# Kernel tuning notes

Hardware: AMD Instinct MI355X
Metric: run time of the kernel (lower is better)

Reference implementation:

```python
import jax, jax.numpy as jnp
import numpy as np

B, S, H, U = 32, 4096, 512, 512


def setup_inputs() -> dict:
    key = jax.random.key(0)
    ks = jax.random.split(key, 6)
    scale = 1.0 / np.sqrt(H)
    return {
        "query": jax.random.normal(ks[0], (B, H), dtype=jnp.float32),
        "values": jax.random.normal(ks[1], (B, S, H), dtype=jnp.float32),
        "W1": jax.random.normal(ks[2], (H, U), dtype=jnp.float32) * scale,
        "b1": jnp.zeros((U,), dtype=jnp.float32),
        "W2": jax.random.normal(ks[3], (H, U), dtype=jnp.float32) * scale,
        "b2": jnp.zeros((U,), dtype=jnp.float32),
        "va": jax.random.normal(ks[4], (U, 1), dtype=jnp.float32) * (1.0 / np.sqrt(U)),
        "bva": jnp.zeros((1,), dtype=jnp.float32),
    }


def reference(query, values, W1, b1, W2, b2, va, bva):
    # query: [B, H] -> [B, 1, U]; values: [B, S, H] -> [B, S, U]
    q_proj = jnp.einsum('bh,hu->bu', query, W1) + b1           # [B, U]
    v_proj = jnp.einsum('bsh,hu->bsu', values, W2) + b2        # [B, S, U]
    scores = jnp.einsum('bsu,uo->bso', jnp.tanh(q_proj[:, None, :] + v_proj), va) + bva  # [B, S, 1]
    attention_weights = jax.nn.softmax(scores, axis=1)         # [B, S, 1]
    context_vector = jnp.sum(attention_weights * values, axis=1)  # [B, H]
    return attention_weights, context_vector
```

## Files before the change

### kernel.cpp

```cpp
#include <hip/hip_runtime.h>
#include <hip/hip_bf16.h>
#include <stdint.h>

#define B_SZ 32
#define S_SZ 4096
#define H_SZ 512
#define U_SZ 512

typedef __attribute__((ext_vector_type(8))) _Float16 half8;
typedef __attribute__((ext_vector_type(4))) float floatx4;

__device__ __forceinline__ void async_copy16(const void* g, void* l) {
    __builtin_amdgcn_global_load_lds(
        (const __attribute__((address_space(1))) void*)g,
        (__attribute__((address_space(3))) void*)l, 16, 0, 0);
}

__global__ __launch_bounds__(256) void prep_kernel(
    const float* __restrict__ W2, _Float16* __restrict__ W2s,
    float* __restrict__ qpb2, float* __restrict__ ctx)
{
    const int t = threadIdx.x;
    const int bid = blockIdx.x;
    const int i = bid * 256 + t;
    const int k = i >> 9, n = i & 511;
    W2s[(k >> 5) * 16384 + ((k >> 3) & 3) * 4096 + n * 8 + (k & 7)] =
        (_Float16)W2[i];
    if (bid < 64) qpb2[i] = 0.0f;
    else if (bid < 128) ctx[(bid - 64) * 256 + t] = 0.0f;
}

__global__ __launch_bounds__(256) void qproj_kernel(
    const float* __restrict__ query, const float* __restrict__ W1,
    const float* __restrict__ b1, const float* __restrict__ b2,
    float* __restrict__ qpb2)
{
    const int b = blockIdx.x, uc = blockIdx.y, ks = blockIdx.z;
    const int u = uc * 256 + threadIdx.x;
    float acc = (ks == 0) ? (b1[u] + b2[u]) : 0.0f;
    const float* q  = query + b * H_SZ + ks * 128;
    const float* Wp = W1 + (size_t)(ks * 128) * U_SZ + u;
    for (int k = 0; k < 128; ++k)
        acc = fmaf(q[k], Wp[(size_t)k * U_SZ], acc);
    atomicAdd(&qpb2[b * U_SZ + u], acc);
}

__global__ __launch_bounds__(256, 2) void scores_kernel(
    const float* __restrict__ values, const _Float16* __restrict__ W2s,
    const float* __restrict__ qpb2, const float* __restrict__ va,
    const float* __restrict__ bva, float* __restrict__ scores)
{
    __shared__ __align__(16) char smem[65536];

    const int t  = threadIdx.x;
    const int w  = t >> 6;
    const int l  = t & 63;
    const int c  = l & 15;
    const int g4 = l >> 4;
    const int m0 = blockIdx.x * 64;
    const int b  = m0 >> 12;

    const float* Abase = values + (size_t)m0 * H_SZ;

    floatx4 acc[4][8];
#pragma unroll
    for (int mt = 0; mt < 4; ++mt)
#pragma unroll
        for (int nt = 0; nt < 8; ++nt) acc[mt][nt] = (floatx4)(0.0f);

    {
        const char* src = (const char*)W2s;
#pragma unroll
        for (int i = 0; i < 8; ++i)
            async_copy16(src + (i * 256 + t) * 16, smem + (i * 256 + t) * 16);
    }
    float4 Apre[4][2];
    {
        const int ko = g4 * 8;
#pragma unroll
        for (int mt = 0; mt < 4; ++mt) {
            const float* ap = Abase + (size_t)(mt * 16 + c) * H_SZ + ko;
            Apre[mt][0] = *(const float4*)(ap);
            Apre[mt][1] = *(const float4*)(ap + 4);
        }
    }
    __syncthreads();

    for (int kb = 0; kb < 16; ++kb) {
        const int cur = kb & 1;
        half8 af[4];
#pragma unroll
        for (int mt = 0; mt < 4; ++mt) {
            half8 a;
            a[0] = (_Float16)Apre[mt][0].x; a[1] = (_Float16)Apre[mt][0].y;
            a[2] = (_Float16)Apre[mt][0].z; a[3] = (_Float16)Apre[mt][0].w;
            a[4] = (_Float16)Apre[mt][1].x; a[5] = (_Float16)Apre[mt][1].y;
            a[6] = (_Float16)Apre[mt][1].z; a[7] = (_Float16)Apre[mt][1].w;
            af[mt] = a;
        }
        if (kb < 15) {
            const int ko = (kb + 1) * 32 + g4 * 8;
#pragma unroll
            for (int mt = 0; mt < 4; ++mt) {
                const float* ap = Abase + (size_t)(mt * 16 + c) * H_SZ + ko;
                Apre[mt][0] = *(const float4*)(ap);
                Apre[mt][1] = *(const float4*)(ap + 4);
            }
            const char* src = (const char*)W2s + (size_t)(kb + 1) * 32768;
            char* dst = smem + (cur ^ 1) * 32768;
#pragma unroll
            for (int i = 0; i < 8; ++i)
                async_copy16(src + (i * 256 + t) * 16, dst + (i * 256 + t) * 16);
        }
        const _Float16* Bc = (const _Float16*)(smem + cur * 32768);
        half8 bf[8];
#pragma unroll
        for (int nt = 0; nt < 8; ++nt)
            bf[nt] = *(const half8*)(Bc + g4 * 4096 + (w * 128 + nt * 16 + c) * 8);
#pragma unroll
        for (int mt = 0; mt < 4; ++mt)
#pragma unroll
            for (int nt = 0; nt < 8; ++nt)
                acc[mt][nt] = __builtin_amdgcn_mfma_f32_16x16x32_f16(
                    af[mt], bf[nt], acc[mt][nt], 0, 0, 0);
        __syncthreads();
    }

    float qv2[8], vv[8], vv2[8];
#pragma unroll
    for (int nt = 0; nt < 8; ++nt) {
        const int n = w * 128 + nt * 16 + c;
        const float q = qpb2[b * U_SZ + n];
        const float v = va[n];
        qv2[nt] = 2.0f * q;
        vv[nt] = v;
        vv2[nt] = 2.0f * v;
    }
    float* red = (float*)smem;
#pragma unroll
    for (int mt = 0; mt < 4; ++mt) {
#pragma unroll
        for (int r = 0; r < 4; ++r) {
            float p = 0.0f;
#pragma unroll
            for (int nt = 0; nt < 8; ++nt) {
                const float ex = __expf(fmaf(acc[mt][nt][r], 2.0f, qv2[nt]));
                const float rc = __builtin_amdgcn_rcpf(ex + 1.0f);
                p = fmaf(-vv2[nt], rc, p + vv[nt]);
            }
            p += __shfl_xor(p, 1);
            p += __shfl_xor(p, 2);
            p += __shfl_xor(p, 4);
            p += __shfl_xor(p, 8);
            if (c == 0) red[(mt * 16 + g4 * 4 + r) * 4 + w] = p;
        }
    }
    __syncthreads();
    if (t < 64)
        scores[m0 + t] = *bva + red[t * 4 + 0] + red[t * 4 + 1] +
                         red[t * 4 + 2] + red[t * 4 + 3];
}

__global__ __launch_bounds__(1024) void sredux_kernel(
    const float* __restrict__ scores, float* __restrict__ ML)
{
    __shared__ float red[16];
    __shared__ float s_max;
    const int b = blockIdx.x;
    const int t = threadIdx.x;
    float4 v = *(const float4*)(scores + b * S_SZ + t * 4);
    float m = fmaxf(fmaxf(v.x, v.y), fmaxf(v.z, v.w));
#pragma unroll
    for (int o = 32; o > 0; o >>= 1) m = fmaxf(m, __shfl_xor(m, o));
    if ((t & 63) == 0) red[t >> 6] = m;
    __syncthreads();
    if (t == 0) {
        float mm = red[0];
        for (int i = 1; i < 16; ++i) mm = fmaxf(mm, red[i]);
        s_max = mm;
    }
    __syncthreads();
    const float mm = s_max;
    float s = __expf(v.x - mm) + __expf(v.y - mm) +
              __expf(v.z - mm) + __expf(v.w - mm);
#pragma unroll
    for (int o = 32; o > 0; o >>= 1) s += __shfl_xor(s, o);
    if ((t & 63) == 0) red[t >> 6] = s;
    __syncthreads();
    if (t == 0) {
        float ss = 0.0f;
        for (int i = 0; i < 16; ++i) ss += red[i];
        ML[b * 2] = mm;
        ML[b * 2 + 1] = ss;
    }
}

__global__ __launch_bounds__(256) void context_kernel(
    const float* __restrict__ values, const float* __restrict__ scores,
    const float* __restrict__ ML, float* __restrict__ out)
{
    __shared__ float wl[256];
    __shared__ __align__(16) float part[4][64][4];
    const int ss = blockIdx.x, hc = blockIdx.y, b = blockIdx.z;
    const int t = threadIdx.x;
    const float M = ML[b * 2];
    const float rL = 1.0f / ML[b * 2 + 1];
    const int s = ss * 256 + t;
    const float wv = __expf(scores[b * S_SZ + s] - M) * rL;
    wl[t] = wv;
    if (hc == 0) out[b * S_SZ + s] = wv;
    __syncthreads();

    const int l = t & 63, g = t >> 6;
    const int h = hc * 256 + l * 4;
    const float* vp = values + ((size_t)b * S_SZ + ss * 256 + g * 64) * H_SZ + h;
    float4 a0 = {0.f, 0.f, 0.f, 0.f}, a1 = {0.f, 0.f, 0.f, 0.f};
    for (int i = 0; i < 64; i += 2) {
        const float w0 = wl[g * 64 + i];
        const float w1 = wl[g * 64 + i + 1];
        float4 v0 = *(const float4*)(vp + (size_t)i * H_SZ);
        float4 v1 = *(const float4*)(vp + (size_t)(i + 1) * H_SZ);
        a0.x = fmaf(w0, v0.x, a0.x); a0.y = fmaf(w0, v0.y, a0.y);
        a0.z = fmaf(w0, v0.z, a0.z); a0.w = fmaf(w0, v0.w, a0.w);
        a1.x = fmaf(w1, v1.x, a1.x); a1.y = fmaf(w1, v1.y, a1.y);
        a1.z = fmaf(w1, v1.z, a1.z); a1.w = fmaf(w1, v1.w, a1.w);
    }
    a0.x += a1.x; a0.y += a1.y; a0.z += a1.z; a0.w += a1.w;
    *(float4*)&part[g][l][0] = a0;
    __syncthreads();
    if (t < 64) {
        float4 sa = *(float4*)&part[0][t][0];
#pragma unroll
        for (int gg = 1; gg < 4; ++gg) {
            float4 p = *(float4*)&part[gg][t][0];
            sa.x += p.x; sa.y += p.y; sa.z += p.z; sa.w += p.w;
        }
        float* ctx = out + B_SZ * S_SZ;
        const int hh = hc * 256 + t * 4;
        atomicAdd(&ctx[b * H_SZ + hh + 0], sa.x);
        atomicAdd(&ctx[b * H_SZ + hh + 1], sa.y);
        atomicAdd(&ctx[b * H_SZ + hh + 2], sa.z);
        atomicAdd(&ctx[b * H_SZ + hh + 3], sa.w);
    }
}

extern "C" void kernel_launch(void* const* d_in, const int* in_sizes, int n_in,
                              void* d_out, int out_size, void* d_ws, size_t ws_size,
                              hipStream_t stream) {
    const float* query  = (const float*)d_in[0];
    const float* values = (const float*)d_in[1];
    const float* W1     = (const float*)d_in[2];
    const float* b1     = (const float*)d_in[3];
    const float* W2     = (const float*)d_in[4];
    const float* b2     = (const float*)d_in[5];
    const float* va     = (const float*)d_in[6];
    const float* bva    = (const float*)d_in[7];
    float* out = (float*)d_out;

    char* ws = (char*)d_ws;
    float*    qpb2   = (float*)ws;
    _Float16* W2s    = (_Float16*)(ws + 65536);
    float*    scores = (float*)(ws + 65536 + 524288);
    float*    ML     = (float*)(ws + 65536 + 524288 + 524288);

    float* ctx = out + B_SZ * S_SZ;

    prep_kernel<<<1024, 256, 0, stream>>>(W2, W2s, qpb2, ctx);
    qproj_kernel<<<dim3(32, 2, 4), 256, 0, stream>>>(query, W1, b1, b2, qpb2);
    scores_kernel<<<2048, 256, 0, stream>>>(values, W2s, qpb2, va, bva, scores);
    sredux_kernel<<<32, 1024, 0, stream>>>(scores, ML);
    context_kernel<<<dim3(16, 2, 32), 256, 0, stream>>>(values, scores, ML, out);
}
```

Before: 545.9 us.

## Drop LDS staging of W2 in scores GEMM, retune qproj and context grids

The scores kernel no longer stages W2 tiles in shared memory with async copies and barriers. Each wave now loads its B fragments straight from global memory (L2-resident) and prefetches the next A tile in registers, which frees 64KB of LDS and removes per-iteration syncs. The qproj kernel splits K across 8 blocks with 4 independent accumulators, and the context kernel uses twice as many blocks, each covering 128 rows with 4-way unrolled loads. Risks are redundant global traffic for W2 across waves and blocks, and more atomics in the context reduction.

```diff
diff --git a/kernel.cpp b/kernel.cpp
--- a/kernel.cpp
+++ b/kernel.cpp
@@ -9,12 +9,6 @@
 
 typedef __attribute__((ext_vector_type(8))) _Float16 half8;
 typedef __attribute__((ext_vector_type(4))) float floatx4;
-
-__device__ __forceinline__ void async_copy16(const void* g, void* l) {
-    __builtin_amdgcn_global_load_lds(
-        (const __attribute__((address_space(1))) void*)g,
-        (__attribute__((address_space(3))) void*)l, 16, 0, 0);
-}
 
 __global__ __launch_bounds__(256) void prep_kernel(
     const float* __restrict__ W2, _Float16* __restrict__ W2s,
@@ -37,11 +31,17 @@
 {
     const int b = blockIdx.x, uc = blockIdx.y, ks = blockIdx.z;
     const int u = uc * 256 + threadIdx.x;
-    float acc = (ks == 0) ? (b1[u] + b2[u]) : 0.0f;
-    const float* q  = query + b * H_SZ + ks * 128;
-    const float* Wp = W1 + (size_t)(ks * 128) * U_SZ + u;
-    for (int k = 0; k < 128; ++k)
-        acc = fmaf(q[k], Wp[(size_t)k * U_SZ], acc);
+    const float* q  = query + b * H_SZ + ks * 64;
+    const float* Wp = W1 + (size_t)(ks * 64) * U_SZ + u;
+    float a0 = 0.f, a1 = 0.f, a2 = 0.f, a3 = 0.f;
+    for (int k = 0; k < 64; k += 4) {
+        a0 = fmaf(q[k],     Wp[(size_t)k * U_SZ],       a0);
+        a1 = fmaf(q[k + 1], Wp[(size_t)(k + 1) * U_SZ], a1);
+        a2 = fmaf(q[k + 2], Wp[(size_t)(k + 2) * U_SZ], a2);
+        a3 = fmaf(q[k + 3], Wp[(size_t)(k + 3) * U_SZ], a3);
+    }
+    float acc = (a0 + a1) + (a2 + a3);
+    if (ks == 0) acc += b1[u] + b2[u];
     atomicAdd(&qpb2[b * U_SZ + u], acc);
 }
 
@@ -50,7 +50,7 @@
     const float* __restrict__ qpb2, const float* __restrict__ va,
     const float* __restrict__ bva, float* __restrict__ scores)
 {
-    __shared__ __align__(16) char smem[65536];
+    __shared__ float red[256];
 
     const int t  = threadIdx.x;
     const int w  = t >> 6;
@@ -60,70 +60,64 @@
     const int m0 = blockIdx.x * 64;
     const int b  = m0 >> 12;
 
-    const float* Abase = values + (size_t)m0 * H_SZ;
-
     floatx4 acc[4][8];
 #pragma unroll
     for (int mt = 0; mt < 4; ++mt)
 #pragma unroll
         for (int nt = 0; nt < 8; ++nt) acc[mt][nt] = (floatx4)(0.0f);
 
-    {
-        const char* src = (const char*)W2s;
-#pragma unroll
-        for (int i = 0; i < 8; ++i)
-            async_copy16(src + (i * 256 + t) * 16, smem + (i * 256 + t) * 16);
-    }
-    float4 Apre[4][2];
-    {
-        const int ko = g4 * 8;
-#pragma unroll
-        for (int mt = 0; mt < 4; ++mt) {
-            const float* ap = Abase + (size_t)(mt * 16 + c) * H_SZ + ko;
-            Apre[mt][0] = *(const float4*)(ap);
-            Apre[mt][1] = *(const float4*)(ap + 4);
-        }
-    }
-    __syncthreads();
+    const float* Ab = values + (size_t)(m0 + c) * H_SZ + g4 * 8;
+    const _Float16* Bb = W2s + g4 * 4096 + (w * 128 + c) * 8;
+
+    float4 an0[4], an1[4];
+#pragma unroll
+    for (int mt = 0; mt < 4; ++mt) {
+        const float* ap = Ab + (size_t)(mt * 16) * H_SZ;
+        an0[mt] = *(const float4*)(ap);
+        an1[mt] = *(const float4*)(ap + 4);
+    }
+    half8 af[4];
+#pragma unroll
+    for (int mt = 0; mt < 4; ++mt) {
+        half8 a;
+        a[0] = (_Float16)an0[mt].x; a[1] = (_Float16)an0[mt].y;
+        a[2] = (_Float16)an0[mt].z; a[3] = (_Float16)an0[mt].w;
+        a[4] = (_Float16)an1[mt].x; a[5] = (_Float16)an1[mt].y;
+        a[6] = (_Float16)an1[mt].z; a[7] = (_Float16)an1[mt].w;
+        af[mt] = a;
+    }
 
     for (int kb = 0; kb < 16; ++kb) {
-        const int cur = kb & 1;
-        half8 af[4];
-#pragma unroll
-        for (int mt = 0; mt < 4; ++mt) {
-            half8 a;
-            a[0] = (_Float16)Apre[mt][0].x; a[1] = (_Float16)Apre[mt][0].y;
-            a[2] = (_Float16)Apre[mt][0].z; a[3] = (_Float16)Apre[mt][0].w;
-            a[4] = (_Float16)Apre[mt][1].x; a[5] = (_Float16)Apre[mt][1].y;
-            a[6] = (_Float16)Apre[mt][1].z; a[7] = (_Float16)Apre[mt][1].w;
-            af[mt] = a;
-        }
+        half8 bf[8];
+        const _Float16* Bp = Bb + kb * 16384;
+#pragma unroll
+        for (int nt = 0; nt < 8; ++nt)
+            bf[nt] = *(const half8*)(Bp + nt * 128);
         if (kb < 15) {
-            const int ko = (kb + 1) * 32 + g4 * 8;
 #pragma unroll
             for (int mt = 0; mt < 4; ++mt) {
-                const float* ap = Abase + (size_t)(mt * 16 + c) * H_SZ + ko;
-                Apre[mt][0] = *(const float4*)(ap);
-                Apre[mt][1] = *(const float4*)(ap + 4);
+                const float* ap = Ab + (size_t)(mt * 16) * H_SZ + (kb + 1) * 32;
+                an0[mt] = *(const float4*)(ap);
+                an1[mt] = *(const float4*)(ap + 4);
             }
-            const char* src = (const char*)W2s + (size_t)(kb + 1) * 32768;
-            char* dst = smem + (cur ^ 1) * 32768;
-#pragma unroll
-            for (int i = 0; i < 8; ++i)
-                async_copy16(src + (i * 256 + t) * 16, dst + (i * 256 + t) * 16);
-        }
-        const _Float16* Bc = (const _Float16*)(smem + cur * 32768);
-        half8 bf[8];
+        }
 #pragma unroll
         for (int nt = 0; nt < 8; ++nt)
-            bf[nt] = *(const half8*)(Bc + g4 * 4096 + (w * 128 + nt * 16 + c) * 8);
-#pragma unroll
-        for (int mt = 0; mt < 4; ++mt)
-#pragma unroll
-            for (int nt = 0; nt < 8; ++nt)
+#pragma unroll
+            for (int mt = 0; mt < 4; ++mt)
                 acc[mt][nt] = __builtin_amdgcn_mfma_f32_16x16x32_f16(
                     af[mt], bf[nt], acc[mt][nt], 0, 0, 0);
-        __syncthreads();
+        if (kb < 15) {
+#pragma unroll
+            for (int mt = 0; mt < 4; ++mt) {
+                half8 a;
+                a[0] = (_Float16)an0[mt].x; a[1] = (_Float16)an0[mt].y;
+                a[2] = (_Float16)an0[mt].z; a[3] = (_Float16)an0[mt].w;
+                a[4] = (_Float16)an1[mt].x; a[5] = (_Float16)an1[mt].y;
+                a[6] = (_Float16)an1[mt].z; a[7] = (_Float16)an1[mt].w;
+                af[mt] = a;
+            }
+        }
     }
 
     float qv2[8], vv[8], vv2[8];
@@ -136,7 +130,6 @@
         vv[nt] = v;
         vv2[nt] = 2.0f * v;
     }
-    float* red = (float*)smem;
 #pragma unroll
     for (int mt = 0; mt < 4; ++mt) {
 #pragma unroll
@@ -199,33 +192,47 @@
     const float* __restrict__ values, const float* __restrict__ scores,
     const float* __restrict__ ML, float* __restrict__ out)
 {
-    __shared__ float wl[256];
+    __shared__ float wl[128];
     __shared__ __align__(16) float part[4][64][4];
     const int ss = blockIdx.x, hc = blockIdx.y, b = blockIdx.z;
     const int t = threadIdx.x;
     const float M = ML[b * 2];
     const float rL = 1.0f / ML[b * 2 + 1];
-    const int s = ss * 256 + t;
-    const float wv = __expf(scores[b * S_SZ + s] - M) * rL;
-    wl[t] = wv;
-    if (hc == 0) out[b * S_SZ + s] = wv;
+    if (t < 32) {
+        float4 sv = *(const float4*)(scores + b * S_SZ + ss * 128 + t * 4);
+        float4 wv;
+        wv.x = __expf(sv.x - M) * rL; wv.y = __expf(sv.y - M) * rL;
+        wv.z = __expf(sv.z - M) * rL; wv.w = __expf(sv.w - M) * rL;
+        *(float4*)&wl[t * 4] = wv;
+        if (hc == 0)
+            *(float4*)(out + b * S_SZ + ss * 128 + t * 4) = wv;
+    }
     __syncthreads();
 
     const int l = t & 63, g = t >> 6;
-    const int h = hc * 256 + l * 4;
-    const float* vp = values + ((size_t)b * S_SZ + ss * 256 + g * 64) * H_SZ + h;
-    float4 a0 = {0.f, 0.f, 0.f, 0.f}, a1 = {0.f, 0.f, 0.f, 0.f};
-    for (int i = 0; i < 64; i += 2) {
-        const float w0 = wl[g * 64 + i];
-        const float w1 = wl[g * 64 + i + 1];
-        float4 v0 = *(const float4*)(vp + (size_t)i * H_SZ);
+    const float* vp = values + ((size_t)b * S_SZ + ss * 128 + g * 32) * H_SZ +
+                      hc * 256 + l * 4;
+    float4 a0 = {0,0,0,0}, a1 = {0,0,0,0}, a2 = {0,0,0,0}, a3 = {0,0,0,0};
+    for (int i = 0; i < 32; i += 4) {
+        const float w0 = wl[g * 32 + i];
+        const float w1 = wl[g * 32 + i + 1];
+        const float w2 = wl[g * 32 + i + 2];
+        const float w3 = wl[g * 32 + i + 3];
+        float4 v0 = *(const float4*)(vp + (size_t)(i)     * H_SZ);
         float4 v1 = *(const float4*)(vp + (size_t)(i + 1) * H_SZ);
+        float4 v2 = *(const float4*)(vp + (size_t)(i + 2) * H_SZ);
+        float4 v3 = *(const float4*)(vp + (size_t)(i + 3) * H_SZ);
         a0.x = fmaf(w0, v0.x, a0.x); a0.y = fmaf(w0, v0.y, a0.y);
         a0.z = fmaf(w0, v0.z, a0.z); a0.w = fmaf(w0, v0.w, a0.w);
         a1.x = fmaf(w1, v1.x, a1.x); a1.y = fmaf(w1, v1.y, a1.y);
         a1.z = fmaf(w1, v1.z, a1.z); a1.w = fmaf(w1, v1.w, a1.w);
-    }
-    a0.x += a1.x; a0.y += a1.y; a0.z += a1.z; a0.w += a1.w;
+        a2.x = fmaf(w2, v2.x, a2.x); a2.y = fmaf(w2, v2.y, a2.y);
+        a2.z = fmaf(w2, v2.z, a2.z); a2.w = fmaf(w2, v2.w, a2.w);
+        a3.x = fmaf(w3, v3.x, a3.x); a3.y = fmaf(w3, v3.y, a3.y);
+        a3.z = fmaf(w3, v3.z, a3.z); a3.w = fmaf(w3, v3.w, a3.w);
+    }
+    a0.x += a1.x + a2.x + a3.x; a0.y += a1.y + a2.y + a3.y;
+    a0.z += a1.z + a2.z + a3.z; a0.w += a1.w + a2.w + a3.w;
     *(float4*)&part[g][l][0] = a0;
     __syncthreads();
     if (t < 64) {
@@ -266,8 +273,8 @@
     float* ctx = out + B_SZ * S_SZ;
 
     prep_kernel<<<1024, 256, 0, stream>>>(W2, W2s, qpb2, ctx);
-    qproj_kernel<<<dim3(32, 2, 4), 256, 0, stream>>>(query, W1, b1, b2, qpb2);
+    qproj_kernel<<<dim3(32, 2, 8), 256, 0, stream>>>(query, W1, b1, b2, qpb2);
     scores_kernel<<<2048, 256, 0, stream>>>(values, W2s, qpb2, va, bva, scores);
     sredux_kernel<<<32, 1024, 0, stream>>>(scores, ML);
-    context_kernel<<<dim3(16, 2, 32), 256, 0, stream>>>(values, scores, ML, out);
-}
+    context_kernel<<<dim3(32, 2, 32), 256, 0, stream>>>(values, scores, ML, out);
+}
```

Result: slower. 618.0 us (+13.2%).
